# Optimization experiments

Hardware: AMD Instinct MI355X
Metric: run time of the kernel (lower is better)

## Reference

```python
import jax, jax.numpy as jnp
import numpy as np

N_NODES = 100000
N_EDGES = 640000
D_FEAT = 128
UNITS = 128


def setup_inputs() -> dict:
    key = jax.random.key(0)
    k1, k2, k3, k4, k5 = jax.random.split(key, 5)
    X = jax.random.normal(k1, (N_NODES, D_FEAT), dtype=jnp.float32)
    ref_A = jax.random.randint(k2, (N_EDGES,), 0, N_NODES, dtype=jnp.int32)
    ref_B = jax.random.randint(k3, (N_EDGES,), 0, N_NODES, dtype=jnp.int32)
    # GlorotUniform-style params (scale approximated; exact init irrelevant for math)
    limit_w = np.sqrt(6.0 / (D_FEAT + UNITS)).astype(np.float32)
    w = jax.random.uniform(k4, (D_FEAT, UNITS), minval=-limit_w, maxval=limit_w, dtype=jnp.float32)
    b = jax.random.uniform(k5, (UNITS,), minval=-0.1, maxval=0.1, dtype=jnp.float32)
    return {"X": X, "ref_A": ref_A, "ref_B": ref_B, "w": w, "b": b}


def reference(X, ref_A, ref_B, w, b):
    # c.convolution: gather source-node features along edges, scatter-add to
    # destination nodes (sum aggregation over incoming messages).
    msgs = X[ref_A]                                        # [E, D]
    agg = jax.ops.segment_sum(msgs, ref_B, num_segments=X.shape[0])  # [N, D]
    out = agg @ w + b                                      # [N, units]
    return out
```

## Files before the change

kernel.cpp:

```cpp
#include <hip/hip_runtime.h>
#include <hip/hip_bf16.h>

typedef short s16x8 __attribute__((ext_vector_type(8)));
typedef float f32x4 __attribute__((ext_vector_type(4)));

static __device__ inline unsigned short f2bf(float f) {
    __hip_bfloat16 h = __float2bfloat16(f);
    return *reinterpret_cast<unsigned short*>(&h);
}


__global__ __launch_bounds__(256) void hist_kernel(
    const int* __restrict__ B, int* __restrict__ hist, int E)
{
    int e = blockIdx.x * 256 + threadIdx.x;
    if (e < E) atomicAdd(&hist[B[e]], 1);
}

__global__ __launch_bounds__(256) void scan1_kernel(
    const int* __restrict__ hist, int* __restrict__ offsets,
    int* __restrict__ blockSums, int N)
{
    __shared__ int s[256];
    int tid = threadIdx.x;
    int i = blockIdx.x * 256 + tid;
    int v = (i < N) ? hist[i] : 0;
    s[tid] = v;
    __syncthreads();
    for (int off = 1; off < 256; off <<= 1) {
        int t = (tid >= off) ? s[tid - off] : 0;
        __syncthreads();
        s[tid] += t;
        __syncthreads();
    }
    if (i < N) offsets[i] = s[tid] - v;
    if (tid == 255) blockSums[blockIdx.x] = s[255];
}

__global__ __launch_bounds__(512) void scan2_kernel(
    int* __restrict__ blockSums, int nb)
{
    __shared__ int s[512];
    int tid = threadIdx.x;
    int v = (tid < nb) ? blockSums[tid] : 0;
    s[tid] = v;
    __syncthreads();
    for (int off = 1; off < 512; off <<= 1) {
        int t = (tid >= off) ? s[tid - off] : 0;
        __syncthreads();
        s[tid] += t;
        __syncthreads();
    }
    if (tid < nb) blockSums[tid] = s[tid] - v;
}

__global__ __launch_bounds__(256) void scan3_kernel(
    int* __restrict__ offsets, int* __restrict__ cursor,
    const int* __restrict__ blockSums, int N)
{
    int i = blockIdx.x * 256 + threadIdx.x;
    if (i < N) {
        int o = offsets[i] + blockSums[blockIdx.x];
        offsets[i] = o;
        cursor[i]  = o;
    }
}

__global__ __launch_bounds__(256) void fill_kernel(
    const int* __restrict__ A, const int* __restrict__ B,
    int* __restrict__ cursor, int* __restrict__ csr_src, int E)
{
    int e = blockIdx.x * 256 + threadIdx.x;
    if (e < E) {
        int pos = atomicAdd(&cursor[B[e]], 1);
        csr_src[pos] = A[e];
    }
}

__global__ __launch_bounds__(256) void wtrans_kernel(
    const float* __restrict__ w, unsigned short* __restrict__ wT)
{
    int i = blockIdx.x * 256 + threadIdx.x;
    int n = i >> 7, k = i & 127;
    wT[i] = f2bf(w[k * 128 + n]);
}

__global__ __launch_bounds__(256) void agg_kernel(
    const float* __restrict__ X, const int* __restrict__ offsets,
    const int* __restrict__ ends, const int* __restrict__ csr_src,
    unsigned short* __restrict__ aggb, int N)
{
    int g = blockIdx.x * 256 + threadIdx.x;
    int node = g >> 6;
    if (node >= N) return;
    int lane = g & 63;

    int s = offsets[node];
    int e = ends[node];
    int deg = e - s;

    int idx = s + lane;
    int src_l = (idx < e) ? csr_src[idx] : 0;

    float2 acc = make_float2(0.f, 0.f);
    for (int j = 0; j < deg; ++j) {
        int jm = j & 63;
        if (j != 0 && jm == 0) {
            idx += 64;
            src_l = (idx < e) ? csr_src[idx] : 0;
        }
        int src = __shfl(src_l, jm);
        float2 v = *(const float2*)(X + (size_t)src * 128 + lane * 2);
        acc.x += v.x; acc.y += v.y;
    }

    unsigned int pk = (unsigned int)f2bf(acc.x) | ((unsigned int)f2bf(acc.y) << 16);
    *(unsigned int*)(aggb + (size_t)node * 128 + lane * 2) = pk;
}

__global__ __launch_bounds__(256) void gemm_mfma_kernel(
    const unsigned short* __restrict__ aggb, const unsigned short* __restrict__ wT,
    const float* __restrict__ b, float* __restrict__ out, int N)
{
    const int tid  = threadIdx.x;
    const int wave = tid >> 6;
    const int lane = tid & 63;
    const int m = lane & 15;
    const int q = lane >> 4;

    const int row0 = blockIdx.x * 64 + wave * 16;

    int arow = row0 + m;
    if (arow >= N) arow = N - 1;
    const unsigned short* abase = aggb + (size_t)arow * 128 + q * 8;

    s16x8 a[4];
    #pragma unroll
    for (int s = 0; s < 4; ++s)
        a[s] = *(const s16x8*)(abase + s * 32);

    f32x4 acc[8] = {};
    #pragma unroll
    for (int s = 0; s < 4; ++s) {
        #pragma unroll
        for (int c = 0; c < 8; ++c) {
            s16x8 bf = *(const s16x8*)&wT[(size_t)(c * 16 + m) * 128 + s * 32 + q * 8];
            acc[c] = __builtin_amdgcn_mfma_f32_16x16x32_bf16(a[s], bf, acc[c], 0, 0, 0);
        }
    }

    const int r0 = row0 + q * 4;
    #pragma unroll
    for (int c = 0; c < 8; ++c) {
        int col = c * 16 + m;
        float bias = b[col];
        #pragma unroll
        for (int r = 0; r < 4; ++r) {
            int row = r0 + r;
            if (row < N)
                out[(size_t)row * 128 + col] = acc[c][r] + bias;
        }
    }
}

extern "C" void kernel_launch(void* const* d_in, const int* in_sizes, int n_in,
                              void* d_out, int out_size, void* d_ws, size_t ws_size,
                              hipStream_t stream) {
    const float* X = (const float*)d_in[0];
    const int*   A = (const int*)d_in[1];
    const int*   B = (const int*)d_in[2];
    const float* w = (const float*)d_in[3];
    const float* b = (const float*)d_in[4];
    float* out = (float*)d_out;

    const int N = in_sizes[0] / 128;
    const int E = in_sizes[1];

    char* wsb = (char*)d_ws;
    size_t off = 0;
    int* hist      = (int*)(wsb + off); off += (size_t)4 * N;
    int* offsets   = (int*)(wsb + off); off += (size_t)4 * N;
    int* cursor    = (int*)(wsb + off); off += (size_t)4 * N;
    int* blockSums = (int*)(wsb + off); off += 2048;
    unsigned short* wT = (unsigned short*)(wsb + off); off += 32768;
    off = (off + 255) & ~(size_t)255;
    unsigned short* aggb = (unsigned short*)(wsb + off); off += (size_t)N * 256;
    off = (off + 255) & ~(size_t)255;
    int* csr_src   = (int*)(wsb + off);

    const int nbN = (N + 255) / 256;
    const int nbE = (E + 255) / 256;

    hipMemsetAsync(hist, 0, (size_t)4 * N, stream);
    hist_kernel<<<nbE, 256, 0, stream>>>(B, hist, E);
    scan1_kernel<<<nbN, 256, 0, stream>>>(hist, offsets, blockSums, N);
    scan2_kernel<<<1, 512, 0, stream>>>(blockSums, nbN);
    scan3_kernel<<<nbN, 256, 0, stream>>>(offsets, cursor, blockSums, N);
    fill_kernel<<<nbE, 256, 0, stream>>>(A, B, cursor, csr_src, E);
    wtrans_kernel<<<64, 256, 0, stream>>>(w, wT);

    {
        long threads = (long)N * 64;
        int grid = (int)((threads + 255) / 256);
        agg_kernel<<<grid, 256, 0, stream>>>(X, offsets, cursor, csr_src, aggb, N);
    }
    {
        int grid = (N + 63) / 64;
        gemm_mfma_kernel<<<grid, 256, 0, stream>>>(aggb, wT, b, out, N);
    }
}
```

Baseline: 265.4 us.

## Fuse aggregation with MFMA GEMM, gather bf16 X, and drop scan3 pass

Converts X to packed bf16 in a prep kernel that also transposes w and zeroes the histogram, which halves the bytes read per gathered row. The scan3 pass is removed: fill and aggregation add the block prefix on the fly and derive each segment's start from its end minus its degree. Aggregation and GEMM become a single kernel in which each wave aggregates 16 nodes into LDS and then runs MFMA straight from LDS, so the aggb round-trip through global memory goes away. Costs are an extra full pass over X for the conversion, sums of bf16-rounded inputs, and a sequential per-wave node loop that may lower occupancy and latency hiding.

```diff
diff --git a/kernel.cpp b/kernel.cpp
--- a/kernel.cpp
+++ b/kernel.cpp
@@ -9,6 +9,22 @@
     return *reinterpret_cast<unsigned short*>(&h);
 }
 
+__global__ __launch_bounds__(256) void prep_kernel(
+    const float* __restrict__ X, const float* __restrict__ w,
+    unsigned int* __restrict__ Xb, unsigned short* __restrict__ wT,
+    int* __restrict__ hist, int N, int nx2)
+{
+    int i = blockIdx.x * 256 + threadIdx.x;
+    if (i < nx2) {
+        float2 v = ((const float2*)X)[i];
+        Xb[i] = (unsigned int)f2bf(v.x) | ((unsigned int)f2bf(v.y) << 16);
+    }
+    if (i < 16384) {
+        int n = i >> 7, k = i & 127;
+        wT[i] = f2bf(w[k * 128 + n]);
+    }
+    if (i < N) hist[i] = 0;
+}
 
 __global__ __launch_bounds__(256) void hist_kernel(
     const int* __restrict__ B, int* __restrict__ hist, int E)
@@ -18,7 +34,7 @@
 }
 
 __global__ __launch_bounds__(256) void scan1_kernel(
-    const int* __restrict__ hist, int* __restrict__ offsets,
+    const int* __restrict__ hist, int* __restrict__ cursor,
     int* __restrict__ blockSums, int N)
 {
     __shared__ int s[256];
@@ -33,7 +49,7 @@
         s[tid] += t;
         __syncthreads();
     }
-    if (i < N) offsets[i] = s[tid] - v;
+    if (i < N) cursor[i] = s[tid] - v;
     if (tid == 255) blockSums[blockIdx.x] = s[255];
 }
 
@@ -54,90 +70,75 @@
     if (tid < nb) blockSums[tid] = s[tid] - v;
 }
 
-__global__ __launch_bounds__(256) void scan3_kernel(
-    int* __restrict__ offsets, int* __restrict__ cursor,
-    const int* __restrict__ blockSums, int N)
-{
-    int i = blockIdx.x * 256 + threadIdx.x;
-    if (i < N) {
-        int o = offsets[i] + blockSums[blockIdx.x];
-        offsets[i] = o;
-        cursor[i]  = o;
-    }
-}
-
 __global__ __launch_bounds__(256) void fill_kernel(
     const int* __restrict__ A, const int* __restrict__ B,
-    int* __restrict__ cursor, int* __restrict__ csr_src, int E)
+    int* __restrict__ cursor, const int* __restrict__ blockSums,
+    int* __restrict__ csr_src, int E)
 {
     int e = blockIdx.x * 256 + threadIdx.x;
     if (e < E) {
-        int pos = atomicAdd(&cursor[B[e]], 1);
+        int d = B[e];
+        int pos = atomicAdd(&cursor[d], 1) + blockSums[d >> 8];
         csr_src[pos] = A[e];
     }
 }
 
-__global__ __launch_bounds__(256) void wtrans_kernel(
-    const float* __restrict__ w, unsigned short* __restrict__ wT)
-{
-    int i = blockIdx.x * 256 + threadIdx.x;
-    int n = i >> 7, k = i & 127;
-    wT[i] = f2bf(w[k * 128 + n]);
-}
-
-__global__ __launch_bounds__(256) void agg_kernel(
-    const float* __restrict__ X, const int* __restrict__ offsets,
-    const int* __restrict__ ends, const int* __restrict__ csr_src,
-    unsigned short* __restrict__ aggb, int N)
-{
-    int g = blockIdx.x * 256 + threadIdx.x;
-    int node = g >> 6;
-    if (node >= N) return;
-    int lane = g & 63;
-
-    int s = offsets[node];
-    int e = ends[node];
-    int deg = e - s;
-
-    int idx = s + lane;
-    int src_l = (idx < e) ? csr_src[idx] : 0;
-
-    float2 acc = make_float2(0.f, 0.f);
-    for (int j = 0; j < deg; ++j) {
-        int jm = j & 63;
-        if (j != 0 && jm == 0) {
-            idx += 64;
-            src_l = (idx < e) ? csr_src[idx] : 0;
+__global__ __launch_bounds__(256) void aggemm_kernel(
+    const unsigned int* __restrict__ Xb, const int* __restrict__ hist,
+    const int* __restrict__ cursor, const int* __restrict__ bs,
+    const int* __restrict__ csr_src, const unsigned short* __restrict__ wT,
+    const float* __restrict__ b, float* __restrict__ out, int N)
+{
+    __shared__ unsigned int lds[64 * 68];
+
+    const int tid  = threadIdx.x;
+    const int w    = tid >> 6;
+    const int lane = tid & 63;
+    const int m    = lane & 15;
+    const int q    = lane >> 4;
+    const int row0 = blockIdx.x * 64;
+
+    #pragma unroll 1
+    for (int t = 0; t < 16; ++t) {
+        const int lrow = w * 16 + t;
+        const int node = row0 + lrow;
+        float ax = 0.f, ay = 0.f;
+        if (node < N) {
+            int deg = hist[node];
+            int e   = cursor[node] + bs[node >> 8];
+            int s   = e - deg;
+            for (int base = s; base < e; base += 64) {
+                int cnt = e - base; if (cnt > 64) cnt = 64;
+                int idx = base + lane;
+                int src_l = (idx < e) ? csr_src[idx] : 0;
+                int j = 0;
+                for (; j + 1 < cnt; j += 2) {
+                    int s0 = __shfl(src_l, j);
+                    int s1 = __shfl(src_l, j + 1);
+                    unsigned p0 = Xb[(size_t)s0 * 64 + lane];
+                    unsigned p1 = Xb[(size_t)s1 * 64 + lane];
+                    ax += __uint_as_float(p0 << 16);
+                    ay += __uint_as_float(p0 & 0xFFFF0000u);
+                    ax += __uint_as_float(p1 << 16);
+                    ay += __uint_as_float(p1 & 0xFFFF0000u);
+                }
+                if (j < cnt) {
+                    int s0 = __shfl(src_l, j);
+                    unsigned p0 = Xb[(size_t)s0 * 64 + lane];
+                    ax += __uint_as_float(p0 << 16);
+                    ay += __uint_as_float(p0 & 0xFFFF0000u);
+                }
+            }
         }
-        int src = __shfl(src_l, jm);
-        float2 v = *(const float2*)(X + (size_t)src * 128 + lane * 2);
-        acc.x += v.x; acc.y += v.y;
-    }
-
-    unsigned int pk = (unsigned int)f2bf(acc.x) | ((unsigned int)f2bf(acc.y) << 16);
-    *(unsigned int*)(aggb + (size_t)node * 128 + lane * 2) = pk;
-}
-
-__global__ __launch_bounds__(256) void gemm_mfma_kernel(
-    const unsigned short* __restrict__ aggb, const unsigned short* __restrict__ wT,
-    const float* __restrict__ b, float* __restrict__ out, int N)
-{
-    const int tid  = threadIdx.x;
-    const int wave = tid >> 6;
-    const int lane = tid & 63;
-    const int m = lane & 15;
-    const int q = lane >> 4;
-
-    const int row0 = blockIdx.x * 64 + wave * 16;
-
-    int arow = row0 + m;
-    if (arow >= N) arow = N - 1;
-    const unsigned short* abase = aggb + (size_t)arow * 128 + q * 8;
-
+        lds[lrow * 68 + lane] =
+            (unsigned int)f2bf(ax) | ((unsigned int)f2bf(ay) << 16);
+    }
+
+    const unsigned int* arow = &lds[(w * 16 + m) * 68 + q * 4];
     s16x8 a[4];
     #pragma unroll
     for (int s = 0; s < 4; ++s)
-        a[s] = *(const s16x8*)(abase + s * 32);
+        a[s] = *(const s16x8*)(arow + s * 16);
 
     f32x4 acc[8] = {};
     #pragma unroll
@@ -149,7 +150,7 @@
         }
     }
 
-    const int r0 = row0 + q * 4;
+    const int r0 = row0 + w * 16 + q * 4;
     #pragma unroll
     for (int c = 0; c < 8; ++c) {
         int col = c * 16 + m;
@@ -179,33 +180,22 @@
     char* wsb = (char*)d_ws;
     size_t off = 0;
     int* hist      = (int*)(wsb + off); off += (size_t)4 * N;
-    int* offsets   = (int*)(wsb + off); off += (size_t)4 * N;
     int* cursor    = (int*)(wsb + off); off += (size_t)4 * N;
     int* blockSums = (int*)(wsb + off); off += 2048;
     unsigned short* wT = (unsigned short*)(wsb + off); off += 32768;
     off = (off + 255) & ~(size_t)255;
-    unsigned short* aggb = (unsigned short*)(wsb + off); off += (size_t)N * 256;
-    off = (off + 255) & ~(size_t)255;
+    unsigned int* Xb = (unsigned int*)(wsb + off); off += (size_t)N * 256;
     int* csr_src   = (int*)(wsb + off);
 
+    const int nx2 = N * 64;
     const int nbN = (N + 255) / 256;
     const int nbE = (E + 255) / 256;
 
-    hipMemsetAsync(hist, 0, (size_t)4 * N, stream);
+    prep_kernel<<<(nx2 + 255) / 256, 256, 0, stream>>>(X, w, Xb, wT, hist, N, nx2);
     hist_kernel<<<nbE, 256, 0, stream>>>(B, hist, E);
-    scan1_kernel<<<nbN, 256, 0, stream>>>(hist, offsets, blockSums, N);
+    scan1_kernel<<<nbN, 256, 0, stream>>>(hist, cursor, blockSums, N);
     scan2_kernel<<<1, 512, 0, stream>>>(blockSums, nbN);
-    scan3_kernel<<<nbN, 256, 0, stream>>>(offsets, cursor, blockSums, N);
-    fill_kernel<<<nbE, 256, 0, stream>>>(A, B, cursor, csr_src, E);
-    wtrans_kernel<<<64, 256, 0, stream>>>(w, wT);
-
-    {
-        long threads = (long)N * 64;
-        int grid = (int)((threads + 255) / 256);
-        agg_kernel<<<grid, 256, 0, stream>>>(X, offsets, cursor, csr_src, aggb, N);
-    }
-    {
-        int grid = (N + 63) / 64;
-        gemm_mfma_kernel<<<grid, 256, 0, stream>>>(aggb, wT, b, out, N);
-    }
-}
+    fill_kernel<<<nbE, 256, 0, stream>>>(A, B, cursor, blockSums, csr_src, E);
+    aggemm_kernel<<<(N + 63) / 64, 256, 0, stream>>>(
+        Xb, hist, cursor, blockSums, csr_src, wT, b, out, N);
+}
```

After: 282.2 us. 1.06x slower.
